# Kernel tuning notes

Measured on AMD Instinct MI355X. Metric: run time of the kernel, lower is better.

The kernel has to match this reference:

```python
import jax, jax.numpy as jnp
import numpy as np

B, C, I, H, T = 256, 16, 64, 40, 512


def setup_inputs() -> dict:
    key = jax.random.key(0)
    ks = jax.random.split(key, 7)
    s = 1.0 / np.sqrt(H)  # PyTorch GRU/Linear init scale
    return {
        "x": jax.random.normal(ks[0], (B, C, I, T), jnp.float32),
        "W_ih": jax.random.uniform(ks[1], (C, 3 * H, I), jnp.float32, -s, s),
        "W_hh": jax.random.uniform(ks[2], (C, 3 * H, H), jnp.float32, -s, s),
        "b_ih": jax.random.uniform(ks[3], (C, 3 * H), jnp.float32, -s, s),
        "b_hh": jax.random.uniform(ks[4], (C, 3 * H), jnp.float32, -s, s),
        "W_fc": jax.random.uniform(ks[5], (C, 1, H), jnp.float32, -s, s),
        "b_fc": jax.random.uniform(ks[6], (C, 1), jnp.float32, -s, s),
    }


def reference(x, W_ih, W_hh, b_ih, b_hh, W_fc, b_fc):
    # x: [B, C, I, T] -> time-major [T, B, C, I] (module permutes to batch_first [B,T,I] per channel)
    xt = jnp.transpose(x, (3, 0, 1, 2))
    hid = W_hh.shape[-1]
    # Precompute input projections for all steps/channels at once: [T, B, C, 3H]
    gi = jnp.einsum('tbci,cgi->tbcg', xt, W_ih) + b_ih

    def step(h, gi_t):
        # h: [B, C, H]
        gh = jnp.einsum('bch,cgh->bcg', h, W_hh) + b_hh  # [B, C, 3H]
        i_r, i_z, i_n = jnp.split(gi_t, 3, axis=-1)
        h_r, h_z, h_n = jnp.split(gh, 3, axis=-1)
        r = jax.nn.sigmoid(i_r + h_r)
        z = jax.nn.sigmoid(i_z + h_z)
        n = jnp.tanh(i_n + r * h_n)
        h_new = (1.0 - z) * n + z * h
        return h_new, None

    h0 = jnp.zeros((x.shape[0], x.shape[1], hid), x.dtype)
    h_final, _ = jax.lax.scan(step, h0, gi)  # final hidden [B, C, H]

    # Channel-wise FC (H -> 1) + sigmoid: [B, C, 1]
    y = jnp.einsum('bch,coh->bco', h_final, W_fc) + b_fc
    return jax.nn.sigmoid(y)
```

## Files before the change

### kernel.cpp

```cpp
#include <hip/hip_runtime.h>

#define B_ 256
#define C_ 16
#define I_ 64
#define H_ 40
#define T_ 512
#define G_ 120

#define TT  16
#define NCH (T_ / TT)
#define NT  640

#define SX  72
#define SG  132
#define SH  132
#define SHB 72

typedef short bf16x8 __attribute__((ext_vector_type(8)));
typedef float f32x4  __attribute__((ext_vector_type(4)));

__device__ __forceinline__ unsigned short f2bf(float f) {
    unsigned u = __float_as_uint(f);
    unsigned r = (u + 0x7FFFu + ((u >> 16) & 1u)) >> 16;
    return (unsigned short)r;
}
__device__ __forceinline__ float bf2f(unsigned s) {
    return __uint_as_float(s << 16);
}
__device__ __forceinline__ float sigf(float x) {
    return 1.0f / (1.0f + __expf(-x));
}

__global__ __launch_bounds__(NT, 1)
void gru_mfma_kernel(const float* __restrict__ x,
                     const float* __restrict__ Wih,
                     const float* __restrict__ Whh,
                     const float* __restrict__ bih,
                     const float* __restrict__ bhh,
                     const float* __restrict__ Wfc,
                     const float* __restrict__ bfc,
                     float* __restrict__ out)
{
    __shared__ __align__(16) unsigned short xa[256 * SX];
    __shared__ __align__(16) unsigned short gi_buf[256 * SG];
    __shared__ __align__(16) float          gh_buf[16 * SH];
    __shared__ __align__(16) unsigned short hbf[16 * SHB];

    const int tid = threadIdx.x;
    const int c   = blockIdx.x >> 4;
    const int b0  = (blockIdx.x & 15) * 16;
    const int wav = tid >> 6;
    const int lan = tid & 63;
    const int lq  = lan >> 4;
    const int lm  = lan & 15;

    const int rb = tid & 15;
    const int rk = tid >> 4;

    float hreg = 0.0f;
    for (int idx = tid; idx < 16 * SHB; idx += NT) hbf[idx] = 0;

    bf16x8 wihf[2], whhf[2];
    f32x4 bias4 = {0.f, 0.f, 0.f, 0.f};
    if (wav < 8) {
        const int g = wav * 16 + lm;
        #pragma unroll
        for (int ks = 0; ks < 2; ++ks) {
            bf16x8 a, b;
            #pragma unroll
            for (int j = 0; j < 8; ++j) {
                int kk = ks * 32 + lq * 8 + j;
                float wi = (g < G_) ? Wih[((size_t)c * G_ + g) * I_ + kk] : 0.0f;
                float wh = (g < G_ && kk < H_) ? Whh[((size_t)c * G_ + g) * H_ + kk] : 0.0f;
                a[j] = (short)f2bf(wi);
                b[j] = (short)f2bf(wh);
            }
            wihf[ks] = a;
            whhf[ks] = b;
        }
        float bb[4];
        #pragma unroll
        for (int r = 0; r < 4; ++r) {
            int gg = wav * 16 + lq * 4 + r;
            float v = 0.0f;
            if (gg < 80)      v = bih[c * G_ + gg] + bhh[c * G_ + gg];
            else if (gg < G_) v = bhh[c * G_ + gg];
            bb[r] = v;
        }
        bias4 = {bb[0], bb[1], bb[2], bb[3]};
    }

    const float bihn = bih[c * G_ + 80 + rk];
    const float wfck = Wfc[c * H_ + rk];

    float4 pf[7];
    #define PREFETCH(T0)                                                           \
        {                                                                          \
            _Pragma("unroll")                                                      \
            for (int it = 0; it < 7; ++it) {                                       \
                int idx = tid + it * NT;                                           \
                if (idx < 4096) {                                                  \
                    int q = idx & 3, i = (idx >> 2) & 63, b = idx >> 8;            \
                    const float* p = x + ((((size_t)(b0 + b) * C_ + c) * I_ + i)   \
                                          * T_ + (T0) + q * 4);                    \
                    pf[it] = *reinterpret_cast<const float4*>(p);                  \
                }                                                                  \
            }                                                                      \
        }

    PREFETCH(0);

    for (int ch = 0; ch < NCH; ++ch) {
        #pragma unroll
        for (int it = 0; it < 7; ++it) {
            int idx = tid + it * NT;
            if (idx < 4096) {
                int q = idx & 3, i = (idx >> 2) & 63, b = idx >> 8;
                float4 v = pf[it];
                xa[((q * 4 + 0) * 16 + b) * SX + i] = f2bf(v.x);
                xa[((q * 4 + 1) * 16 + b) * SX + i] = f2bf(v.y);
                xa[((q * 4 + 2) * 16 + b) * SX + i] = f2bf(v.z);
                xa[((q * 4 + 3) * 16 + b) * SX + i] = f2bf(v.w);
            }
        }
        __syncthreads();

        if (wav < 8) {
            #pragma unroll 4
            for (int nt = 0; nt < 16; ++nt) {
                const unsigned short* xp = &xa[(nt * 16 + lm) * SX];
                bf16x8 xb0 = *reinterpret_cast<const bf16x8*>(xp + lq * 8);
                bf16x8 xb1 = *reinterpret_cast<const bf16x8*>(xp + 32 + lq * 8);
                f32x4 acc = {0.f, 0.f, 0.f, 0.f};
                acc = __builtin_amdgcn_mfma_f32_16x16x32_bf16(wihf[0], xb0, acc, 0, 0, 0);
                acc = __builtin_amdgcn_mfma_f32_16x16x32_bf16(wihf[1], xb1, acc, 0, 0, 0);
                unsigned lo = (unsigned)f2bf(acc[0]) | ((unsigned)f2bf(acc[1]) << 16);
                unsigned hi = (unsigned)f2bf(acc[2]) | ((unsigned)f2bf(acc[3]) << 16);
                uint2 val; val.x = lo; val.y = hi;
                *reinterpret_cast<uint2*>(&gi_buf[(nt * 16 + lm) * SG + wav * 16 + lq * 4]) = val;
            }
        }
        __syncthreads();

        {
            int tn = (ch + 1 < NCH) ? (ch + 1) * TT : 0;
            PREFETCH(tn);
        }

        for (int tt = 0; tt < TT; ++tt) {
            if (wav < 8) {
                const unsigned short* hp = &hbf[lm * SHB];
                bf16x8 h0 = *reinterpret_cast<const bf16x8*>(hp + lq * 8);
                bf16x8 h1 = *reinterpret_cast<const bf16x8*>(hp + 32 + lq * 8);
                f32x4 acc = bias4;
                acc = __builtin_amdgcn_mfma_f32_16x16x32_bf16(whhf[0], h0, acc, 0, 0, 0);
                acc = __builtin_amdgcn_mfma_f32_16x16x32_bf16(whhf[1], h1, acc, 0, 0, 0);
                if (wav < 5) {
                    uint2 gv = *reinterpret_cast<const uint2*>(
                        &gi_buf[(tt * 16 + lm) * SG + wav * 16 + lq * 4]);
                    acc[0] += bf2f(gv.x & 0xffffu);
                    acc[1] += bf2f(gv.x >> 16);
                    acc[2] += bf2f(gv.y & 0xffffu);
                    acc[3] += bf2f(gv.y >> 16);
                }
                *reinterpret_cast<f32x4*>(&gh_buf[lm * SH + wav * 16 + lq * 4]) = acc;
            }
            __syncthreads();

            {
                float pre_r = gh_buf[rb * SH + rk];
                float pre_z = gh_buf[rb * SH + 40 + rk];
                float h_n   = gh_buf[rb * SH + 80 + rk];
                float i_n   = bf2f((unsigned)gi_buf[(tt * 16 + rb) * SG + 80 + rk]) + bihn;
                float r = sigf(pre_r);
                float z = sigf(pre_z);
                float nl = i_n + r * h_n;
                float e  = __expf(2.0f * nl);
                float n  = 1.0f - 2.0f / (e + 1.0f);
                hreg = (1.0f - z) * n + z * hreg;
                hbf[rb * SHB + rk] = f2bf(hreg);
            }
            __syncthreads();
        }
    }

    float* red = gh_buf;
    red[tid] = hreg * wfck;
    __syncthreads();
    if (tid < 16) {
        float s = bfc[c];
        #pragma unroll
        for (int k = 0; k < H_; ++k) s += red[k * 16 + tid];
        out[(b0 + tid) * C_ + c] = sigf(s);
    }
}

extern "C" void kernel_launch(void* const* d_in, const int* in_sizes, int n_in,
                              void* d_out, int out_size, void* d_ws, size_t ws_size,
                              hipStream_t stream) {
    const float* x   = (const float*)d_in[0];
    const float* Wih = (const float*)d_in[1];
    const float* Whh = (const float*)d_in[2];
    const float* bih = (const float*)d_in[3];
    const float* bhh = (const float*)d_in[4];
    const float* Wfc = (const float*)d_in[5];
    const float* bfc = (const float*)d_in[6];
    float* out = (float*)d_out;

    dim3 grid(C_ * (B_ / 16));
    dim3 block(NT);
    gru_mfma_kernel<<<grid, block, 0, stream>>>(x, Wih, Whh, bih, bhh, Wfc, bfc, out);
}
```

Measured before the change: 964.6 us.

## Interleave gate rows so each lane owns r,z,n for one hidden unit

```diff
diff --git a/kernel.cpp b/kernel.cpp
--- a/kernel.cpp
+++ b/kernel.cpp
@@ -12,8 +12,6 @@
 #define NT  640
 
 #define SX  72
-#define SG  132
-#define SH  132
 #define SHB 72
 
 typedef short bf16x8 __attribute__((ext_vector_type(8)));
@@ -28,7 +26,7 @@
     return __uint_as_float(s << 16);
 }
 __device__ __forceinline__ float sigf(float x) {
-    return 1.0f / (1.0f + __expf(-x));
+    return __builtin_amdgcn_rcpf(1.0f + __expf(-x));
 }
 
 __global__ __launch_bounds__(NT, 1)
@@ -42,73 +40,83 @@
                      float* __restrict__ out)
 {
     __shared__ __align__(16) unsigned short xa[256 * SX];
-    __shared__ __align__(16) unsigned short gi_buf[256 * SG];
-    __shared__ __align__(16) float          gh_buf[16 * SH];
-    __shared__ __align__(16) unsigned short hbf[16 * SHB];
+    __shared__ __align__(16) unsigned short hbf[2][16 * SHB];
 
     const int tid = threadIdx.x;
     const int c   = blockIdx.x >> 4;
     const int b0  = (blockIdx.x & 15) * 16;
-    const int wav = tid >> 6;
+    const int w   = tid >> 6;
     const int lan = tid & 63;
     const int lq  = lan >> 4;
     const int lm  = lan & 15;
-
-    const int rb = tid & 15;
-    const int rk = tid >> 4;
+    const int k   = w * 4 + lq;
+
+    for (int idx = tid; idx < 2 * 16 * SHB; idx += NT)
+        ((unsigned short*)hbf)[idx] = 0;
 
     float hreg = 0.0f;
-    for (int idx = tid; idx < 16 * SHB; idx += NT) hbf[idx] = 0;
+
+    float4 pf[7];
+#define PREFETCH(T0)                                                           \
+    {                                                                          \
+        _Pragma("unroll")                                                      \
+        for (int it = 0; it < 7; ++it) {                                       \
+            int idx = tid + it * NT;                                           \
+            if (idx < 4096) {                                                  \
+                int q = idx & 3, i = (idx >> 2) & 63, b = idx >> 8;            \
+                const float* p = x + ((((size_t)(b0 + b) * C_ + c) * I_ + i)   \
+                                      * T_ + (T0) + q * 4);                    \
+                pf[it] = *reinterpret_cast<const float4*>(p);                  \
+            }                                                                  \
+        }                                                                      \
+    }
+
+    PREFETCH(0);
 
     bf16x8 wihf[2], whhf[2];
-    f32x4 bias4 = {0.f, 0.f, 0.f, 0.f};
-    if (wav < 8) {
-        const int g = wav * 16 + lm;
+    {
+        const int p  = w * 16 + lm;
+        const int pg = p & 3;
+        const int pk = p >> 2;
         #pragma unroll
         for (int ks = 0; ks < 2; ++ks) {
-            bf16x8 a, b;
-            #pragma unroll
-            for (int j = 0; j < 8; ++j) {
-                int kk = ks * 32 + lq * 8 + j;
-                float wi = (g < G_) ? Wih[((size_t)c * G_ + g) * I_ + kk] : 0.0f;
-                float wh = (g < G_ && kk < H_) ? Whh[((size_t)c * G_ + g) * H_ + kk] : 0.0f;
-                a[j] = (short)f2bf(wi);
-                b[j] = (short)f2bf(wh);
+            bf16x8 a  = {0,0,0,0,0,0,0,0};
+            bf16x8 hh = {0,0,0,0,0,0,0,0};
+            if (pg < 3) {
+                const float* wp = Wih + ((size_t)c * G_ + pg * H_ + pk) * I_ + ks * 32 + lq * 8;
+                float4 v0 = *reinterpret_cast<const float4*>(wp);
+                float4 v1 = *reinterpret_cast<const float4*>(wp + 4);
+                a[0]=(short)f2bf(v0.x); a[1]=(short)f2bf(v0.y);
+                a[2]=(short)f2bf(v0.z); a[3]=(short)f2bf(v0.w);
+                a[4]=(short)f2bf(v1.x); a[5]=(short)f2bf(v1.y);
+                a[6]=(short)f2bf(v1.z); a[7]=(short)f2bf(v1.w);
+                if (ks == 0 || lq == 0) {
+                    const float* hp = Whh + ((size_t)c * G_ + pg * H_ + pk) * H_ + ks * 32 + lq * 8;
+                    float4 u0 = *reinterpret_cast<const float4*>(hp);
+                    float4 u1 = *reinterpret_cast<const float4*>(hp + 4);
+                    hh[0]=(short)f2bf(u0.x); hh[1]=(short)f2bf(u0.y);
+                    hh[2]=(short)f2bf(u0.z); hh[3]=(short)f2bf(u0.w);
+                    hh[4]=(short)f2bf(u1.x); hh[5]=(short)f2bf(u1.y);
+                    hh[6]=(short)f2bf(u1.z); hh[7]=(short)f2bf(u1.w);
+                }
             }
             wihf[ks] = a;
-            whhf[ks] = b;
-        }
-        float bb[4];
-        #pragma unroll
-        for (int r = 0; r < 4; ++r) {
-            int gg = wav * 16 + lq * 4 + r;
-            float v = 0.0f;
-            if (gg < 80)      v = bih[c * G_ + gg] + bhh[c * G_ + gg];
-            else if (gg < G_) v = bhh[c * G_ + gg];
-            bb[r] = v;
-        }
-        bias4 = {bb[0], bb[1], bb[2], bb[3]};
-    }
-
-    const float bihn = bih[c * G_ + 80 + rk];
-    const float wfck = Wfc[c * H_ + rk];
-
-    float4 pf[7];
-    #define PREFETCH(T0)                                                           \
-        {                                                                          \
-            _Pragma("unroll")                                                      \
-            for (int it = 0; it < 7; ++it) {                                       \
-                int idx = tid + it * NT;                                           \
-                if (idx < 4096) {                                                  \
-                    int q = idx & 3, i = (idx >> 2) & 63, b = idx >> 8;            \
-                    const float* p = x + ((((size_t)(b0 + b) * C_ + c) * I_ + i)   \
-                                          * T_ + (T0) + q * 4);                    \
-                    pf[it] = *reinterpret_cast<const float4*>(p);                  \
-                }                                                                  \
-            }                                                                      \
-        }
-
-    PREFETCH(0);
+            whhf[ks] = hh;
+        }
+    }
+
+    f32x4 bias4;
+    #pragma unroll
+    for (int r = 0; r < 4; ++r) {
+        float v = 0.0f;
+        if (r < 3) v  = bhh[c * G_ + r * H_ + k];
+        if (r < 2) v += bih[c * G_ + r * H_ + k];
+        bias4[r] = v;
+    }
+    const float bihn = bih[c * G_ + 2 * H_ + k];
+    const float wfck = Wfc[c * H_ + k];
+
+    uint2 gi_reg[16];
 
     for (int ch = 0; ch < NCH; ++ch) {
         #pragma unroll
@@ -116,81 +124,64 @@
             int idx = tid + it * NT;
             if (idx < 4096) {
                 int q = idx & 3, i = (idx >> 2) & 63, b = idx >> 8;
+                int colp = (((i >> 3) ^ q) << 3) | (i & 7);
                 float4 v = pf[it];
-                xa[((q * 4 + 0) * 16 + b) * SX + i] = f2bf(v.x);
-                xa[((q * 4 + 1) * 16 + b) * SX + i] = f2bf(v.y);
-                xa[((q * 4 + 2) * 16 + b) * SX + i] = f2bf(v.z);
-                xa[((q * 4 + 3) * 16 + b) * SX + i] = f2bf(v.w);
+                unsigned short* xr = &xa[(q * 64 + b) * SX + colp];
+                xr[0]       = f2bf(v.x);
+                xr[16 * SX] = f2bf(v.y);
+                xr[32 * SX] = f2bf(v.z);
+                xr[48 * SX] = f2bf(v.w);
             }
         }
         __syncthreads();
 
-        if (wav < 8) {
-            #pragma unroll 4
-            for (int nt = 0; nt < 16; ++nt) {
-                const unsigned short* xp = &xa[(nt * 16 + lm) * SX];
-                bf16x8 xb0 = *reinterpret_cast<const bf16x8*>(xp + lq * 8);
-                bf16x8 xb1 = *reinterpret_cast<const bf16x8*>(xp + 32 + lq * 8);
-                f32x4 acc = {0.f, 0.f, 0.f, 0.f};
-                acc = __builtin_amdgcn_mfma_f32_16x16x32_bf16(wihf[0], xb0, acc, 0, 0, 0);
-                acc = __builtin_amdgcn_mfma_f32_16x16x32_bf16(wihf[1], xb1, acc, 0, 0, 0);
-                unsigned lo = (unsigned)f2bf(acc[0]) | ((unsigned)f2bf(acc[1]) << 16);
-                unsigned hi = (unsigned)f2bf(acc[2]) | ((unsigned)f2bf(acc[3]) << 16);
-                uint2 val; val.x = lo; val.y = hi;
-                *reinterpret_cast<uint2*>(&gi_buf[(nt * 16 + lm) * SG + wav * 16 + lq * 4]) = val;
-            }
-        }
-        __syncthreads();
-
-        {
-            int tn = (ch + 1 < NCH) ? (ch + 1) * TT : 0;
-            PREFETCH(tn);
-        }
-
+        { int tn = (ch + 1 < NCH) ? (ch + 1) * TT : 0; PREFETCH(tn); }
+
+        #pragma unroll
+        for (int nt = 0; nt < 16; ++nt) {
+            const unsigned short* xp = &xa[(nt * 16 + lm) * SX + ((lq ^ (nt >> 2)) << 3)];
+            bf16x8 xb0 = *reinterpret_cast<const bf16x8*>(xp);
+            bf16x8 xb1 = *reinterpret_cast<const bf16x8*>(xp + 32);
+            f32x4 acc = {0.f, 0.f, 0.f, 0.f};
+            acc = __builtin_amdgcn_mfma_f32_16x16x32_bf16(wihf[0], xb0, acc, 0, 0, 0);
+            acc = __builtin_amdgcn_mfma_f32_16x16x32_bf16(wihf[1], xb1, acc, 0, 0, 0);
+            gi_reg[nt].x = (unsigned)f2bf(acc[0]) | ((unsigned)f2bf(acc[1]) << 16);
+            gi_reg[nt].y = (unsigned)f2bf(acc[2]) | ((unsigned)f2bf(acc[3]) << 16);
+        }
+
+        #pragma unroll
         for (int tt = 0; tt < TT; ++tt) {
-            if (wav < 8) {
-                const unsigned short* hp = &hbf[lm * SHB];
-                bf16x8 h0 = *reinterpret_cast<const bf16x8*>(hp + lq * 8);
-                bf16x8 h1 = *reinterpret_cast<const bf16x8*>(hp + 32 + lq * 8);
-                f32x4 acc = bias4;
-                acc = __builtin_amdgcn_mfma_f32_16x16x32_bf16(whhf[0], h0, acc, 0, 0, 0);
-                acc = __builtin_amdgcn_mfma_f32_16x16x32_bf16(whhf[1], h1, acc, 0, 0, 0);
-                if (wav < 5) {
-                    uint2 gv = *reinterpret_cast<const uint2*>(
-                        &gi_buf[(tt * 16 + lm) * SG + wav * 16 + lq * 4]);
-                    acc[0] += bf2f(gv.x & 0xffffu);
-                    acc[1] += bf2f(gv.x >> 16);
-                    acc[2] += bf2f(gv.y & 0xffffu);
-                    acc[3] += bf2f(gv.y >> 16);
-                }
-                *reinterpret_cast<f32x4*>(&gh_buf[lm * SH + wav * 16 + lq * 4]) = acc;
-            }
+            const unsigned short* hp = &hbf[tt & 1][lm * SHB + lq * 8];
+            bf16x8 h0 = *reinterpret_cast<const bf16x8*>(hp);
+            bf16x8 h1 = {0,0,0,0,0,0,0,0};
+            if (lq == 0)
+                h1 = *reinterpret_cast<const bf16x8*>(&hbf[tt & 1][lm * SHB + 32]);
+            f32x4 a1 = bias4;
+            a1 = __builtin_amdgcn_mfma_f32_16x16x32_bf16(whhf[0], h0, a1, 0, 0, 0);
+            f32x4 a2 = {0.f, 0.f, 0.f, 0.f};
+            a2 = __builtin_amdgcn_mfma_f32_16x16x32_bf16(whhf[1], h1, a2, 0, 0, 0);
+            uint2 gv = gi_reg[tt];
+            float pre_r = a1[0] + a2[0] + bf2f(gv.x & 0xffffu);
+            float pre_z = a1[1] + a2[1] + bf2f(gv.x >> 16);
+            float h_n   = a1[2] + a2[2];
+            float i_n   = bf2f(gv.y & 0xffffu) + bihn;
+            float r = sigf(pre_r);
+            float z = sigf(pre_z);
+            float e = __expf(2.0f * (i_n + r * h_n));
+            float n = 1.0f - 2.0f * __builtin_amdgcn_rcpf(e + 1.0f);
+            hreg = (1.0f - z) * n + z * hreg;
+            hbf[(tt & 1) ^ 1][lm * SHB + k] = f2bf(hreg);
             __syncthreads();
-
-            {
-                float pre_r = gh_buf[rb * SH + rk];
-                float pre_z = gh_buf[rb * SH + 40 + rk];
-                float h_n   = gh_buf[rb * SH + 80 + rk];
-                float i_n   = bf2f((unsigned)gi_buf[(tt * 16 + rb) * SG + 80 + rk]) + bihn;
-                float r = sigf(pre_r);
-                float z = sigf(pre_z);
-                float nl = i_n + r * h_n;
-                float e  = __expf(2.0f * nl);
-                float n  = 1.0f - 2.0f / (e + 1.0f);
-                hreg = (1.0f - z) * n + z * hreg;
-                hbf[rb * SHB + rk] = f2bf(hreg);
-            }
-            __syncthreads();
-        }
-    }
-
-    float* red = gh_buf;
+        }
+    }
+
+    float* red = reinterpret_cast<float*>(xa);
     red[tid] = hreg * wfck;
     __syncthreads();
     if (tid < 16) {
         float s = bfc[c];
         #pragma unroll
-        for (int k = 0; k < H_; ++k) s += red[k * 16 + tid];
+        for (int kk = 0; kk < H_; ++kk) s += red[kk * 16 + tid];
         out[(b0 + tid) * C_ + c] = sigf(s);
     }
 }
```

Result: faster. 803.9 us (-16.7%).
